# Optimization experiments

Measured on AMD Instinct MI355X. Metric: run time of the kernel, lower is better.

Reference implementation:

```python
import jax, jax.numpy as jnp
import numpy as np

B, S, DIM = 4, 3968, 512
H, HD = 8, 64
CHUNK, NPM, MEM = 496, 32, 1024  # MEM == NPM + 2*CHUNK (required by module's EMA update broadcast)


def _lin(k, din, dout):
    kw, kb = jax.random.split(k)
    w = jax.random.normal(kw, (din, dout), jnp.float32) / np.sqrt(din)
    b = jax.random.normal(kb, (dout,), jnp.float32) * 0.01
    return w, b


def setup_inputs() -> dict:
    key = jax.random.key(0)
    ks = jax.random.split(key, 12)
    inp = {}
    inp["x"] = jax.random.normal(ks[0], (B, S, DIM), jnp.float32)
    inp["persistent_memory"] = jax.random.normal(ks[1], (NPM, DIM), jnp.float32)
    # outer query projection
    inp["Wq_out"], inp["bq_out"] = _lin(ks[2], DIM, DIM)
    # NeuralMemory projections
    inp["mk_w"], inp["mk_b"] = _lin(ks[3], DIM, DIM)
    inp["mv_w"], inp["mv_b"] = _lin(ks[4], DIM, DIM)
    inp["mq_w"], inp["mq_b"] = _lin(ks[5], DIM, DIM)
    # TitanAttention (standard MHA: q/k/v to H*HD, out proj back to DIM)
    inp["aq_w"], inp["aq_b"] = _lin(ks[6], DIM, H * HD)
    inp["ak_w"], inp["ak_b"] = _lin(ks[7], DIM, H * HD)
    inp["av_w"], inp["av_b"] = _lin(ks[8], DIM, H * HD)
    inp["ao_w"], inp["ao_b"] = _lin(ks[9], H * HD, DIM)
    return inp


def reference(x, persistent_memory, Wq_out, bq_out,
              mk_w, mk_b, mv_w, mv_b, mq_w, mq_b,
              aq_w, aq_b, ak_w, ak_b, av_w, av_b, ao_w, ao_b):
    Bn, Sn, D = x.shape
    nch = Sn // CHUNK
    inv_sqrt_d = 1.0 / np.sqrt(D).astype(np.float32)
    inv_sqrt_hd = 1.0 / np.sqrt(HD).astype(np.float32)

    def retrieve(mem, q):
        # mem: [B, MEM, D], q: [B, L, D]
        qp = q @ mq_w + mq_b
        k = mem @ mk_w + mk_b
        v = mem @ mv_w + mv_b
        sc = jnp.einsum('bqd,bmd->bqm', qp, k) * inv_sqrt_d
        a = jax.nn.softmax(sc, axis=-1)
        return jnp.einsum('bqm,bmd->bqd', a, v)

    def mha(t):
        # t: [B, L, D] -> [B, L, D]; dropout inactive (eval)
        Bm, L, _ = t.shape
        q = (t @ aq_w + aq_b).reshape(Bm, L, H, HD)
        k = (t @ ak_w + ak_b).reshape(Bm, L, H, HD)
        v = (t @ av_w + av_b).reshape(Bm, L, H, HD)
        sc = jnp.einsum('bqhd,bkhd->bhqk', q, k) * inv_sqrt_hd
        a = jax.nn.softmax(sc, axis=-1)
        o = jnp.einsum('bhqk,bkhd->bqhd', a, v).reshape(Bm, L, H * HD)
        return o @ ao_w + ao_b

    pm = jnp.broadcast_to(persistent_memory[None], (Bn, NPM, D))
    chunks = x.reshape(Bn, nch, CHUNK, D).transpose(1, 0, 2, 3)  # [nch, B, C, D]
    mem0 = jnp.zeros((Bn, MEM, D), x.dtype)

    def step(mem, chunk):
        query = chunk @ Wq_out + bq_out
        hist = retrieve(mem, query)                              # [B, C, D]
        combined = jnp.concatenate([pm, hist, chunk], axis=1)    # [B, MEM, D]
        attended = mha(combined)
        mem2 = 0.9 * mem + 0.1 * attended                        # EMA update
        mout = retrieve(mem2, attended)
        out = (attended * mout)[:, -CHUNK:]                      # keep last chunk slice
        return mem2, out

    _, outs = jax.lax.scan(step, mem0, chunks)                   # outs: [nch, B, C, D]
    return outs.transpose(1, 0, 2, 3).reshape(Bn, Sn, D)
```

## Files before the change

kernel.cpp:

```cpp
#include <hip/hip_runtime.h>
#include <hip/hip_fp16.h>


typedef __attribute__((ext_vector_type(8))) short short8;
typedef __attribute__((ext_vector_type(4))) float f32x4;

static __device__ __forceinline__ unsigned short f32_bf16(float f) {
  unsigned int u = __float_as_uint(f);
  u += 0x7FFFu + ((u >> 16) & 1u);
  return (unsigned short)(u >> 16);
}
static __device__ __forceinline__ unsigned pk(float lo, float hi) {
  return (unsigned)f32_bf16(lo) | ((unsigned)f32_bf16(hi) << 16);
}

template<int BM, int BN, int ATY, int BTY, int CTY, bool GUARD, bool BIAS>
__global__ __launch_bounds__(256) void gemm2(
    const void* __restrict__ Ap, long long Asb, long long Ash, int Ars,
    const void* __restrict__ Bp, long long Bsb, long long Bsh, int Brs,
    void* __restrict__ Cp, long long Csb, long long Csh, int Crs,
    void* __restrict__ Cp2, int csplit, void* __restrict__ Cp3,
    const float* __restrict__ bias, float scale, int M, int Kdim, int Hh)
{
  constexpr int LDP = 72;
  constexpr int WN = (BN >= 128) ? 2 : (BM >= 128 ? 1 : 2);
  constexpr int WM = 4 / WN;
  constexpr int MI = BM / (WM * 16);
  constexpr int NI = BN / (WN * 16);
  constexpr int AP = BM / 32;
  constexpr int BP = BN / 32;

  __shared__ unsigned short As[2][BM][LDP];
  __shared__ unsigned short Bs[2][BN][LDP];

  const int tid  = threadIdx.x;
  const int lane = tid & 63;
  const int w    = tid >> 6;
  const int wm   = w / WN, wn = w % WN;
  const int z    = blockIdx.z;
  const int zb   = z / Hh, zh = z - zb * Hh;
  const int m0   = blockIdx.x * BM;
  const int n0   = blockIdx.y * BN;
  const int lrow = lane & 15;
  const int lkB  = (lane >> 4) * 8;
  const int srow = tid >> 3;
  const int scol = (tid & 7) * 8;

  const float*          Af  = (const float*)Ap          + zb * Asb + zh * Ash;
  const unsigned short* Ahp = (const unsigned short*)Ap + zb * Asb + zh * Ash;
  const float*          Bf  = (const float*)Bp          + zb * Bsb + zh * Bsh;
  const unsigned short* Bhp = (const unsigned short*)Bp + zb * Bsb + zh * Bsh;

  float4 afl[AP][2]; uint4 ahl[AP];
  float4 bfl[BP][2]; uint4 bhl[BP];

  auto loadT = [&](int k0) {
    #pragma unroll
    for (int p = 0; p < AP; ++p) {
      const int row = srow + p * 32;
      const bool ok = !GUARD || (m0 + row) < M;
      if constexpr (ATY == 0) {
        if (ok) {
          const float* s = Af + (long long)(m0 + row) * Ars + k0 + scol;
          afl[p][0] = *(const float4*)s;
          afl[p][1] = *(const float4*)(s + 4);
        } else {
          afl[p][0] = make_float4(0.f,0.f,0.f,0.f);
          afl[p][1] = make_float4(0.f,0.f,0.f,0.f);
        }
      } else {
        ahl[p] = ok ? *(const uint4*)(Ahp + (long long)(m0 + row) * Ars + k0 + scol)
                    : make_uint4(0u,0u,0u,0u);
      }
    }
    #pragma unroll
    for (int p = 0; p < BP; ++p) {
      const int row = srow + p * 32;
      if constexpr (BTY == 0) {
        const float* s = Bf + (long long)(n0 + row) * Brs + k0 + scol;
        bfl[p][0] = *(const float4*)s;
        bfl[p][1] = *(const float4*)(s + 4);
      } else {
        bhl[p] = *(const uint4*)(Bhp + (long long)(n0 + row) * Brs + k0 + scol);
      }
    }
  };
  auto writeT = [&](int buf) {
    #pragma unroll
    for (int p = 0; p < AP; ++p) {
      const int row = srow + p * 32;
      uint4 u;
      if constexpr (ATY == 0) {
        u.x = pk(afl[p][0].x, afl[p][0].y); u.y = pk(afl[p][0].z, afl[p][0].w);
        u.z = pk(afl[p][1].x, afl[p][1].y); u.w = pk(afl[p][1].z, afl[p][1].w);
      } else u = ahl[p];
      *(uint4*)(&As[buf][row][scol]) = u;
    }
    #pragma unroll
    for (int p = 0; p < BP; ++p) {
      const int row = srow + p * 32;
      uint4 u;
      if constexpr (BTY == 0) {
        u.x = pk(bfl[p][0].x, bfl[p][0].y); u.y = pk(bfl[p][0].z, bfl[p][0].w);
        u.z = pk(bfl[p][1].x, bfl[p][1].y); u.w = pk(bfl[p][1].z, bfl[p][1].w);
      } else u = bhl[p];
      *(uint4*)(&Bs[buf][row][scol]) = u;
    }
  };

  f32x4 acc[MI][NI] = {};

  loadT(0);
  writeT(0);
  __syncthreads();

  const int NT = Kdim >> 6;
  int cur = 0;
  for (int t = 0; t < NT; ++t) {
    const bool more = (t + 1) < NT;
    if (more) loadT((t + 1) << 6);

    short8 a8[MI][2], b8[NI][2];
    #pragma unroll
    for (int mi = 0; mi < MI; ++mi) {
      const unsigned short* r = &As[cur][wm * (MI * 16) + mi * 16 + lrow][lkB];
      a8[mi][0] = *(const short8*)r;
      a8[mi][1] = *(const short8*)(r + 32);
    }
    #pragma unroll
    for (int ni = 0; ni < NI; ++ni) {
      const unsigned short* r = &Bs[cur][wn * (NI * 16) + ni * 16 + lrow][lkB];
      b8[ni][0] = *(const short8*)r;
      b8[ni][1] = *(const short8*)(r + 32);
    }
    #pragma unroll
    for (int kk = 0; kk < 2; ++kk)
      #pragma unroll
      for (int mi = 0; mi < MI; ++mi)
        #pragma unroll
        for (int ni = 0; ni < NI; ++ni)
          acc[mi][ni] = __builtin_amdgcn_mfma_f32_16x16x32_bf16(a8[mi][kk], b8[ni][kk], acc[mi][ni], 0, 0, 0);

    if (more) writeT(cur ^ 1);
    __syncthreads();
    cur ^= 1;
  }

  float*          Cf  = (float*)Cp          + zb * Csb + zh * Csh;
  unsigned short* Chn = (unsigned short*)Cp + zb * Csb + zh * Csh;
  unsigned short* Ch2 = (unsigned short*)Cp2;
  unsigned short* Kb3 = (unsigned short*)Cp3;
  const bool trside = (CTY == 4 || CTY == 5) ? (n0 >= csplit) : false;

  #pragma unroll
  for (int ni = 0; ni < NI; ++ni) {
    const int col = n0 + wn * (NI * 16) + ni * 16 + lrow;
    const float bv = BIAS ? bias[col] : 0.0f;
    #pragma unroll
    for (int mi = 0; mi < MI; ++mi) {
      const int rbase = m0 + wm * (MI * 16) + mi * 16 + ((lane >> 4) << 2);
      if constexpr (CTY == 5) {
        ushort4 vt;
        #pragma unroll
        for (int r = 0; r < 4; ++r) {
          const int row = rbase + r;
          const float proj = acc[mi][ni][r] * scale + bv;
          const long long midx = (long long)row * Crs + col;
          const float v = 0.9f * Cf[midx] + 0.1f * proj;
          Cf[midx] = v;
          if (!trside) Kb3[(long long)row * 512 + col] = f32_bf16(v);
          else ((unsigned short*)&vt)[r] = f32_bf16(v);
        }
        if (trside)
          *(ushort4*)(&Ch2[(long long)(rbase >> 10) * 524288
                           + (long long)(col - csplit) * 1024 + (rbase & 1023)]) = vt;
      } else if constexpr (CTY == 6) {
        const float* ATTp = (const float*)Cp2;
        float* Of = (float*)Cp;
        #pragma unroll
        for (int r = 0; r < 4; ++r) {
          const int row = rbase + r;
          if (row < M) {
            const float v = acc[mi][ni][r] * scale;
            const float a = ATTp[((long long)zb * 1024 + 528 + row) * 512 + col];
            Of[((long long)zb * 3968 + (long long)csplit * 496 + row) * 512 + col] = v * a;
          }
        }
      } else if constexpr (CTY == 7) {
        #pragma unroll
        for (int r = 0; r < 4; ++r) {
          const int row = rbase + r;
          const float v = acc[mi][ni][r] * scale + bv;
          Cf[(long long)row * Crs + col] = v;
          Kb3[(long long)row * 512 + col] = f32_bf16(v);
        }
      } else if (trside) {
        ushort4 v;
        v.x = f32_bf16(acc[mi][ni][0] * scale + bv);
        v.y = f32_bf16(acc[mi][ni][1] * scale + bv);
        v.z = f32_bf16(acc[mi][ni][2] * scale + bv);
        v.w = f32_bf16(acc[mi][ni][3] * scale + bv);
        *(ushort4*)(&Ch2[(long long)(rbase >> 10) * 524288
                         + (long long)(col - csplit) * 1024 + (rbase & 1023)]) = v;
      } else {
        #pragma unroll
        for (int r = 0; r < 4; ++r) {
          const int row = rbase + r;
          if (!GUARD || row < M) {
            const float v = acc[mi][ni][r] * scale + bv;
            if constexpr (CTY == 0)      Cf [(long long)row * Crs + col] = v;
            else                         Chn[(long long)row * Crs + col] = f32_bf16(v);
          }
        }
      }
    }
  }
}

__global__ __launch_bounds__(256) void flash_mha(
    const unsigned short* __restrict__ QK, const unsigned short* __restrict__ Vt,
    unsigned short* __restrict__ OH)
{
  __shared__ unsigned short Ks[128][72];
  __shared__ unsigned short Vs[64][136];
  __shared__ unsigned short Ps[64][136];

  const int tid = threadIdx.x, lane = tid & 63, w = tid >> 6;
  const int f = blockIdx.x;
  const int xcd = f & 7, j = f >> 3;
  const int bh = xcd + 8 * (j >> 4);
  const int qt = j & 15;
  const int b = bh >> 3, h = bh & 7;
  const int q0 = qt * 64;
  const unsigned short* Qp = QK + (long long)b * 1048576 + h * 64;
  const unsigned short* Kp = Qp + 512;
  const unsigned short* Vp = Vt + (long long)b * 524288 + (long long)(h * 64) * 1024;
  unsigned short* Op = OH + (long long)b * 524288 + h * 64;

  const int lr = lane & 15, g = lane >> 4, lk = g * 8;
  const int wq = w * 16;

  short8 qb[2];
  qb[0] = *(const short8*)(Qp + (long long)(q0 + wq + lr) * 1024 + lk);
  qb[1] = *(const short8*)(Qp + (long long)(q0 + wq + lr) * 1024 + 32 + lk);

  const int krow = tid >> 1, kcol = (tid & 1) * 32;
  const int vrow = tid >> 2, vcol = (tid & 3) * 32;

  uint4 kl[4], vl[4];
  auto loadKV = [&](int kt) {
    #pragma unroll
    for (int jj = 0; jj < 4; ++jj)
      kl[jj] = *(const uint4*)(Kp + (long long)(kt * 128 + krow) * 1024 + kcol + jj * 8);
    #pragma unroll
    for (int jj = 0; jj < 4; ++jj)
      vl[jj] = *(const uint4*)(Vp + (long long)vrow * 1024 + kt * 128 + vcol + jj * 8);
  };
  auto writeKV = [&]() {
    #pragma unroll
    for (int jj = 0; jj < 4; ++jj) *(uint4*)(&Ks[krow][kcol + jj * 8]) = kl[jj];
    #pragma unroll
    for (int jj = 0; jj < 4; ++jj) *(uint4*)(&Vs[vrow][vcol + jj * 8]) = vl[jj];
  };

  loadKV(0); writeKV();
  __syncthreads();

  f32x4 acc[4] = {};
  float m = -1e30f, l = 0.f;

  for (int kt = 0; kt < 8; ++kt) {
    const bool more = kt < 7;
    if (more) loadKV(kt + 1);

    f32x4 s[8] = {};
    #pragma unroll
    for (int ks = 0; ks < 2; ++ks)
      #pragma unroll
      for (int ni = 0; ni < 8; ++ni) {
        const short8 ka = *(const short8*)(&Ks[ni * 16 + lr][ks * 32 + lk]);
        s[ni] = __builtin_amdgcn_mfma_f32_16x16x32_bf16(ka, qb[ks], s[ni], 0, 0, 0);
      }

    #pragma unroll
    for (int ni = 0; ni < 8; ++ni)
      #pragma unroll
      for (int r = 0; r < 4; ++r) s[ni][r] *= 0.125f;
    f32x4 rv = s[0];
    #pragma unroll
    for (int ni = 1; ni < 8; ++ni)
      #pragma unroll
      for (int r = 0; r < 4; ++r) rv[r] = fmaxf(rv[r], s[ni][r]);
    float rm = fmaxf(fmaxf(rv[0], rv[1]), fmaxf(rv[2], rv[3]));
    rm = fmaxf(rm, __shfl_xor(rm, 16));
    rm = fmaxf(rm, __shfl_xor(rm, 32));

    const float mn = fmaxf(m, rm);
    const float al = __expf(m - mn);
    m = mn;
    f32x4 lv; lv[0] = lv[1] = lv[2] = lv[3] = 0.f;
    #pragma unroll
    for (int ni = 0; ni < 8; ++ni)
      #pragma unroll
      for (int r = 0; r < 4; ++r) { s[ni][r] = __expf(s[ni][r] - m); lv[r] += s[ni][r]; }
    float ls = (lv[0] + lv[1]) + (lv[2] + lv[3]);
    ls += __shfl_xor(ls, 16);
    ls += __shfl_xor(ls, 32);
    l = l * al + ls;
    #pragma unroll
    for (int nd = 0; nd < 4; ++nd)
      #pragma unroll
      for (int r = 0; r < 4; ++r) acc[nd][r] *= al;

    #pragma unroll
    for (int ni = 0; ni < 8; ++ni) {
      unsigned lo, hi;
      asm("v_cvt_pk_bf16_f32 %0, %1, %2" : "=v"(lo) : "v"(s[ni][0]), "v"(s[ni][1]));
      asm("v_cvt_pk_bf16_f32 %0, %1, %2" : "=v"(hi) : "v"(s[ni][2]), "v"(s[ni][3]));
      *(uint2*)(&Ps[wq + lr][ni * 16 + (g << 2)]) = make_uint2(lo, hi);
    }

    #pragma unroll
    for (int ks2 = 0; ks2 < 4; ++ks2) {
      const short8 pb = *(const short8*)(&Ps[wq + lr][ks2 * 32 + lk]);
      #pragma unroll
      for (int nd = 0; nd < 4; ++nd) {
        const short8 va = *(const short8*)(&Vs[nd * 16 + lr][ks2 * 32 + lk]);
        acc[nd] = __builtin_amdgcn_mfma_f32_16x16x32_bf16(va, pb, acc[nd], 0, 0, 0);
      }
    }

    __syncthreads();
    if (more) { writeKV(); __syncthreads(); }
  }

  unsigned short (*Os)[72] = (unsigned short (*)[72])&Ks[0][0];
  const float inv = 1.0f / l;
  #pragma unroll
  for (int nd = 0; nd < 4; ++nd) {
    const float a0 = acc[nd][0] * inv, a1 = acc[nd][1] * inv;
    const float a2 = acc[nd][2] * inv, a3 = acc[nd][3] * inv;
    unsigned lo, hi;
    asm("v_cvt_pk_bf16_f32 %0, %1, %2" : "=v"(lo) : "v"(a0), "v"(a1));
    asm("v_cvt_pk_bf16_f32 %0, %1, %2" : "=v"(hi) : "v"(a2), "v"(a3));
    *(uint2*)(&Os[wq + lr][nd * 16 + (g << 2)]) = make_uint2(lo, hi);
  }
  __syncthreads();
  const int orow = tid >> 2, ocol = (tid & 3) * 16;
  const uint4 u0 = *(const uint4*)(&Os[orow][ocol]);
  const uint4 u1 = *(const uint4*)(&Os[orow][ocol + 8]);
  *(uint4*)(Op + (long long)(q0 + orow) * 512 + ocol) = u0;
  *(uint4*)(Op + (long long)(q0 + orow) * 512 + ocol + 8) = u1;
}

struct TP7 { const float* s[7]; unsigned short* d[7]; };
__global__ __launch_bounds__(256) void transpose7(TP7 tp)
{
  __shared__ float tile[32][33];
  const float* in = tp.s[blockIdx.z];
  unsigned short* out = tp.d[blockIdx.z];
  const int c0 = blockIdx.x * 32, r0 = blockIdx.y * 32;
  const int xx = threadIdx.x & 31, ys = threadIdx.x >> 5;
  #pragma unroll
  for (int yy = ys; yy < 32; yy += 8)
    tile[yy][xx] = in[(long long)(r0 + yy) * 512 + c0 + xx];
  __syncthreads();
  #pragma unroll
  for (int yy = ys; yy < 32; yy += 8)
    out[(long long)(c0 + yy) * 512 + r0 + xx] = f32_bf16(tile[xx][yy]);
}

__global__ __launch_bounds__(256) void softmax_rows_bf(
    const float* __restrict__ buf, unsigned short* __restrict__ obuf,
    int rowsPerZ, long long zStride)
{
  const int gr   = blockIdx.x * 4 + (threadIdx.x >> 6);
  const int lane = threadIdx.x & 63;
  const int z = gr / rowsPerZ;
  const int i = gr - z * rowsPerZ;
  const float* pf = buf + (long long)z * zStride + (long long)i * 1024 + lane * 16;
  float v[16];
  #pragma unroll
  for (int j = 0; j < 4; ++j) {
    const float4 f = ((const float4*)pf)[j];
    v[4*j+0] = f.x; v[4*j+1] = f.y; v[4*j+2] = f.z; v[4*j+3] = f.w;
  }
  float mx = v[0];
  #pragma unroll
  for (int j = 1; j < 16; ++j) mx = fmaxf(mx, v[j]);
  #pragma unroll
  for (int d = 32; d; d >>= 1) mx = fmaxf(mx, __shfl_xor(mx, d));
  float s = 0.0f;
  #pragma unroll
  for (int j = 0; j < 16; ++j) { v[j] = __expf(v[j] - mx); s += v[j]; }
  #pragma unroll
  for (int d = 32; d; d >>= 1) s += __shfl_xor(s, d);
  const float inv = 1.0f / s;
  unsigned short* ph = obuf + (long long)z * zStride + (long long)i * 1024 + lane * 16;
  unsigned uu[8];
  #pragma unroll
  for (int j = 0; j < 8; ++j) uu[j] = pk(v[2*j] * inv, v[2*j+1] * inv);
  ((uint4*)ph)[0] = make_uint4(uu[0], uu[1], uu[2], uu[3]);
  ((uint4*)ph)[1] = make_uint4(uu[4], uu[5], uu[6], uu[7]);
}

__global__ __launch_bounds__(256) void copy_pm_bf(const float* __restrict__ pm, unsigned short* __restrict__ comb)
{
  const int idx = blockIdx.x * 256 + threadIdx.x;
  const int b = idx >> 11, e = idx & 2047;
  const int row = e >> 6, d8 = (e & 63) * 8;
  const float* s = pm + row * 512 + d8;
  const float4 f0 = *(const float4*)s;
  const float4 f1 = *(const float4*)(s + 4);
  uint4 u; u.x = pk(f0.x, f0.y); u.y = pk(f0.z, f0.w); u.z = pk(f1.x, f1.y); u.w = pk(f1.z, f1.w);
  *(uint4*)(comb + (long long)b * 524288 + row * 512 + d8) = u;
}

__global__ __launch_bounds__(256) void copy_chunk_bf(const float* __restrict__ x, unsigned short* __restrict__ comb, int ci)
{
  const int idx = blockIdx.x * 256 + threadIdx.x;
  const int b = idx / 31744, e = idx % 31744;
  const int row = e >> 6, d8 = (e & 63) * 8;
  const float* s = x + ((long long)b * 3968 + ci * 496 + row) * 512 + d8;
  const float4 f0 = *(const float4*)s;
  const float4 f1 = *(const float4*)(s + 4);
  uint4 u; u.x = pk(f0.x, f0.y); u.y = pk(f0.z, f0.w); u.z = pk(f1.x, f1.y); u.w = pk(f1.z, f1.w);
  *(uint4*)(comb + (long long)b * 524288 + (528 + row) * 512 + d8) = u;
}

__global__ __launch_bounds__(256) void init_kv(const float* __restrict__ mkb, const float* __restrict__ mvb,
                                               float* __restrict__ master, unsigned short* __restrict__ Kb)
{
  const int idx = blockIdx.x * 256 + threadIdx.x;
  const int c4 = (idx & 255) * 4;
  const long long row = idx >> 8;
  const float4 v = *(const float4*)((c4 < 512) ? (mkb + c4) : (mvb + c4 - 512));
  *(float4*)(master + row * 1024 + c4) = v;
  if (c4 < 512) {
    ushort4 h; h.x = f32_bf16(v.x); h.y = f32_bf16(v.y); h.z = f32_bf16(v.z); h.w = f32_bf16(v.w);
    *(ushort4*)(Kb + row * 512 + c4) = h;
  }
}

__global__ __launch_bounds__(256) void init_vt(const float* __restrict__ mvb, unsigned short* __restrict__ VT)
{
  const int idx = blockIdx.x * 256 + threadIdx.x;
  const int k8 = (idx & 127) * 8;
  const int d  = (idx >> 7) & 511;
  const int b  = idx >> 16;
  const unsigned short hv = f32_bf16(mvb[d]);
  const ushort4 h4 = make_ushort4(hv, hv, hv, hv);
  unsigned short* dst = VT + (long long)b * 524288 + (long long)d * 1024 + k8;
  *(ushort4*)dst = h4; *(ushort4*)(dst + 4) = h4;
}

__global__ __launch_bounds__(256) void fuse_bias(const float* __restrict__ bq, const float* __restrict__ mq,
                                                 const float* __restrict__ mqb, float* __restrict__ bqm)
{
  const int c = blockIdx.x * 256 + threadIdx.x;
  float s = mqb[c];
  for (int j = 0; j < 512; ++j) s += bq[j] * mq[j * 512 + c];
  bqm[c] = s;
}

extern "C" void kernel_launch(void* const* d_in, const int* in_sizes, int n_in,
                              void* d_out, int out_size, void* d_ws, size_t ws_size,
                              hipStream_t stream)
{
  (void)in_sizes; (void)n_in; (void)out_size; (void)ws_size;
  const float* x   = (const float*)d_in[0];
  const float* pm  = (const float*)d_in[1];
  const float* Wq  = (const float*)d_in[2];
  const float* bq  = (const float*)d_in[3];
  const float* mkw = (const float*)d_in[4];
  const float* mkb = (const float*)d_in[5];
  const float* mvw = (const float*)d_in[6];
  const float* mvb = (const float*)d_in[7];
  const float* mqw = (const float*)d_in[8];
  const float* mqb = (const float*)d_in[9];
  const float* aqw = (const float*)d_in[10];
  const float* aqb = (const float*)d_in[11];
  const float* akw = (const float*)d_in[12];
  const float* akb = (const float*)d_in[13];
  const float* avw = (const float*)d_in[14];
  const float* avb = (const float*)d_in[15];
  const float* aow = (const float*)d_in[16];
  const float* aob = (const float*)d_in[17];
  float* out = (float*)d_out;

  char* wsp = (char*)d_ws;
  size_t off = 0;
  auto alloc = [&](size_t b) -> void* { void* p = wsp + off; off += (b + 255) & ~(size_t)255; return p; };

  unsigned short* WTmq = (unsigned short*)alloc(524288);
  unsigned short* WKV  = (unsigned short*)alloc(1048576);
  unsigned short* WQKV = (unsigned short*)alloc(1572864);
  unsigned short* WTao = (unsigned short*)alloc(524288);
  unsigned short* Wqm  = (unsigned short*)alloc(524288);
  float* bkv  = (float*)alloc(4096);
  float* bqkv = (float*)alloc(6144);
  float* bqm  = (float*)alloc(2048);
  float*          master = (float*)alloc(16777216);
  unsigned short* Kb   = (unsigned short*)alloc(4194304);
  unsigned short* VT   = (unsigned short*)alloc(4194304);
  unsigned short* VTm  = (unsigned short*)alloc(4194304);
  unsigned short* QP1  = (unsigned short*)alloc(16252928);
  unsigned short* QP   = (unsigned short*)alloc(2031616);
  unsigned short* comb = (unsigned short*)alloc(4194304);
  unsigned short* QKb  = (unsigned short*)alloc(8388608);
  unsigned short* OH   = (unsigned short*)alloc(4194304);
  float*          ATT  = (float*)alloc(8388608);
  unsigned short* ATTb = (unsigned short*)alloc(4194304);
  float*          SC   = (float*)alloc(8126464);
  unsigned short* SCb  = (unsigned short*)alloc(4063232);

  const long long XBS = 2031616, BS = 524288, QBS = 253952;
  const long long SCB = 507904;
  const float sr = 0.044194173824159216f;

  TP7 tp;
  tp.s[0] = mqw; tp.d[0] = WTmq;
  tp.s[1] = mkw; tp.d[1] = WKV;
  tp.s[2] = mvw; tp.d[2] = WKV + 262144;
  tp.s[3] = aqw; tp.d[3] = WQKV;
  tp.s[4] = akw; tp.d[4] = WQKV + 262144;
  tp.s[5] = avw; tp.d[5] = WQKV + 524288;
  tp.s[6] = aow; tp.d[6] = WTao;
  transpose7<<<dim3(16,16,7),256,0,stream>>>(tp);
  gemm2<64,64,1,0,2,false,false><<<dim3(8,8,1),256,0,stream>>>(
    WTmq, 0, 0, 512, Wq, 0, 0, 512, Wqm, 0, 0, 512,
    nullptr, 0, nullptr, nullptr, 1.0f, 512, 512, 1);
  fuse_bias<<<2,256,0,stream>>>(bq, mqw, mqb, bqm);
  gemm2<128,64,0,1,2,false,true><<<dim3(124,8,1),256,0,stream>>>(
    x, 0, 0, 512, Wqm, 0, 0, 512,
    QP1, 0, 0, 512, nullptr, 0, nullptr, bqm, 1.0f, 15872, 512, 1);
  hipMemcpyAsync(bkv,        mkb, 2048, hipMemcpyDeviceToDevice, stream);
  hipMemcpyAsync(bkv  + 512, mvb, 2048, hipMemcpyDeviceToDevice, stream);
  hipMemcpyAsync(bqkv,       aqb, 2048, hipMemcpyDeviceToDevice, stream);
  hipMemcpyAsync(bqkv + 512, akb, 2048, hipMemcpyDeviceToDevice, stream);
  hipMemcpyAsync(bqkv +1024, avb, 2048, hipMemcpyDeviceToDevice, stream);
  init_kv<<<4096,256,0,stream>>>(mkb, mvb, master, Kb);
  init_vt<<<1024,256,0,stream>>>(mvb, VT);
  copy_pm_bf<<<32,256,0,stream>>>(pm, comb);

  for (int ci = 0; ci < 8; ++ci) {
    copy_chunk_bf<<<496,256,0,stream>>>(x, comb, ci);

    gemm2<64,64,1,1,0,true,false><<<dim3(8,16,4),256,0,stream>>>(
      QP1 + (long long)ci * 253952, XBS, 0, 512, Kb, BS, 0, 512,
      SC, SCB, 0, 1024, nullptr, 0, nullptr, nullptr, sr, 496, 512, 1);
    softmax_rows_bf<<<496,256,0,stream>>>(SC, SCb, 496, SCB);
    gemm2<64,64,1,1,2,true,false><<<dim3(8,8,4),256,0,stream>>>(
      SCb, SCB, 0, 1024, VT, BS, 0, 1024,
      comb + 32 * 512, BS, 0, 512, nullptr, 0, nullptr, nullptr, 1.0f, 496, 1024, 1);

    gemm2<128,64,1,1,4,false,true><<<dim3(32,24,1),256,0,stream>>>(
      comb, 0, 0, 512, WQKV, 0, 0, 512,
      QKb, 0, 0, 1024, VTm, 1024, nullptr, bqkv, 1.0f, 4096, 512, 1);
    flash_mha<<<512,256,0,stream>>>(QKb, VTm, OH);
    gemm2<128,64,1,1,7,false,true><<<dim3(32,8,1),256,0,stream>>>(
      OH, 0, 0, 512, WTao, 0, 0, 512,
      ATT, 0, 0, 512, nullptr, 0, ATTb, aob, 1.0f, 4096, 512, 1);

    gemm2<128,64,1,1,5,false,true><<<dim3(32,16,1),256,0,stream>>>(
      ATTb, 0, 0, 512, WKV, 0, 0, 512,
      master, 0, 0, 1024, VT, 512, Kb, bkv, 1.0f, 4096, 512, 1);

    gemm2<64,64,1,1,2,true,true><<<dim3(8,8,4),256,0,stream>>>(
      ATTb + 528 * 512, BS, 0, 512, WTmq, 0, 0, 512,
      QP, QBS, 0, 512, nullptr, 0, nullptr, mqb, 1.0f, 496, 512, 1);
    gemm2<64,64,1,1,0,true,false><<<dim3(8,16,4),256,0,stream>>>(
      QP, QBS, 0, 512, Kb, BS, 0, 512,
      SC, SCB, 0, 1024, nullptr, 0, nullptr, nullptr, sr, 496, 512, 1);
    softmax_rows_bf<<<496,256,0,stream>>>(SC, SCb, 496, SCB);
    gemm2<64,64,1,1,6,true,false><<<dim3(8,8,4),256,0,stream>>>(
      SCb, SCB, 0, 1024, VT, BS, 0, 1024,
      out, 0, 0, 512, ATT, ci, nullptr, nullptr, 1.0f, 496, 1024, 1);
  }
}
```

Baseline: 1.336 ms.

## Load K/V MFMA fragments directly from global memory in flash attention, drop LDS staging

The flash attention kernel no longer stages K and V tiles through shared memory with block-wide barriers. Each wave now loads its K and V MFMA operands straight from global memory into registers. The P scratch buffer is shrunk to an unpadded 64x128 array with an XOR swizzle to avoid bank conflicts. This removes the LDS round trip and the __syncthreads per tile, but each of the four waves now fetches the full K/V tile separately, which quadruples global/L2 traffic and raises register pressure, with no prefetch overlap.

New measurement: 1.435 ms. 7.4% more time.

```diff
diff --git a/kernel.cpp b/kernel.cpp
--- a/kernel.cpp
+++ b/kernel.cpp
@@ -221,9 +221,7 @@
     const unsigned short* __restrict__ QK, const unsigned short* __restrict__ Vt,
     unsigned short* __restrict__ OH)
 {
-  __shared__ unsigned short Ks[128][72];
-  __shared__ unsigned short Vs[64][136];
-  __shared__ unsigned short Ps[64][136];
+  __shared__ unsigned short Ps[64][128];
 
   const int tid = threadIdx.x, lane = tid & 63, w = tid >> 6;
   const int f = blockIdx.x;
@@ -239,48 +237,39 @@
 
   const int lr = lane & 15, g = lane >> 4, lk = g * 8;
   const int wq = w * 16;
+  const int swz = (lr & 7) << 4;
+  char* prow = (char*)&Ps[0][0] + (wq + lr) * 256;
 
   short8 qb[2];
   qb[0] = *(const short8*)(Qp + (long long)(q0 + wq + lr) * 1024 + lk);
   qb[1] = *(const short8*)(Qp + (long long)(q0 + wq + lr) * 1024 + 32 + lk);
 
-  const int krow = tid >> 1, kcol = (tid & 1) * 32;
-  const int vrow = tid >> 2, vcol = (tid & 3) * 32;
-
-  uint4 kl[4], vl[4];
-  auto loadKV = [&](int kt) {
-    #pragma unroll
-    for (int jj = 0; jj < 4; ++jj)
-      kl[jj] = *(const uint4*)(Kp + (long long)(kt * 128 + krow) * 1024 + kcol + jj * 8);
-    #pragma unroll
-    for (int jj = 0; jj < 4; ++jj)
-      vl[jj] = *(const uint4*)(Vp + (long long)vrow * 1024 + kt * 128 + vcol + jj * 8);
-  };
-  auto writeKV = [&]() {
-    #pragma unroll
-    for (int jj = 0; jj < 4; ++jj) *(uint4*)(&Ks[krow][kcol + jj * 8]) = kl[jj];
-    #pragma unroll
-    for (int jj = 0; jj < 4; ++jj) *(uint4*)(&Vs[vrow][vcol + jj * 8]) = vl[jj];
-  };
-
-  loadKV(0); writeKV();
-  __syncthreads();
-
   f32x4 acc[4] = {};
   float m = -1e30f, l = 0.f;
 
+  #pragma unroll 1
   for (int kt = 0; kt < 8; ++kt) {
-    const bool more = kt < 7;
-    if (more) loadKV(kt + 1);
+    const unsigned short* kbase = Kp + (long long)(kt * 128 + lr) * 1024 + lk;
+    short8 kf[2][8];
+    #pragma unroll
+    for (int ni = 0; ni < 8; ++ni) {
+      kf[0][ni] = *(const short8*)(kbase + ni * 16384);
+      kf[1][ni] = *(const short8*)(kbase + ni * 16384 + 32);
+    }
+    const unsigned short* vbase = Vp + (long long)lr * 1024 + kt * 128 + lk;
+    short8 vf[4][4];
+    #pragma unroll
+    for (int ks2 = 0; ks2 < 4; ++ks2)
+      #pragma unroll
+      for (int nd = 0; nd < 4; ++nd)
+        vf[ks2][nd] = *(const short8*)(vbase + nd * 16384 + ks2 * 32);
 
     f32x4 s[8] = {};
     #pragma unroll
     for (int ks = 0; ks < 2; ++ks)
       #pragma unroll
-      for (int ni = 0; ni < 8; ++ni) {
-        const short8 ka = *(const short8*)(&Ks[ni * 16 + lr][ks * 32 + lk]);
-        s[ni] = __builtin_amdgcn_mfma_f32_16x16x32_bf16(ka, qb[ks], s[ni], 0, 0, 0);
-      }
+      for (int ni = 0; ni < 8; ++ni)
+        s[ni] = __builtin_amdgcn_mfma_f32_16x16x32_bf16(kf[ks][ni], qb[ks], s[ni], 0, 0, 0);
 
     #pragma unroll
     for (int ni = 0; ni < 8; ++ni)
@@ -317,24 +306,18 @@
       unsigned lo, hi;
       asm("v_cvt_pk_bf16_f32 %0, %1, %2" : "=v"(lo) : "v"(s[ni][0]), "v"(s[ni][1]));
       asm("v_cvt_pk_bf16_f32 %0, %1, %2" : "=v"(hi) : "v"(s[ni][2]), "v"(s[ni][3]));
-      *(uint2*)(&Ps[wq + lr][ni * 16 + (g << 2)]) = make_uint2(lo, hi);
+      *(uint2*)(prow + ((32 * ni + 8 * g) ^ swz)) = make_uint2(lo, hi);
     }
 
     #pragma unroll
     for (int ks2 = 0; ks2 < 4; ++ks2) {
-      const short8 pb = *(const short8*)(&Ps[wq + lr][ks2 * 32 + lk]);
-      #pragma unroll
-      for (int nd = 0; nd < 4; ++nd) {
-        const short8 va = *(const short8*)(&Vs[nd * 16 + lr][ks2 * 32 + lk]);
-        acc[nd] = __builtin_amdgcn_mfma_f32_16x16x32_bf16(va, pb, acc[nd], 0, 0, 0);
-      }
-    }
-
-    __syncthreads();
-    if (more) { writeKV(); __syncthreads(); }
-  }
-
-  unsigned short (*Os)[72] = (unsigned short (*)[72])&Ks[0][0];
+      const short8 pb = *(const short8*)(prow + ((64 * ks2 + 16 * g) ^ swz));
+      #pragma unroll
+      for (int nd = 0; nd < 4; ++nd)
+        acc[nd] = __builtin_amdgcn_mfma_f32_16x16x32_bf16(vf[ks2][nd], pb, acc[nd], 0, 0, 0);
+    }
+  }
+
   const float inv = 1.0f / l;
   #pragma unroll
   for (int nd = 0; nd < 4; ++nd) {
@@ -343,14 +326,16 @@
     unsigned lo, hi;
     asm("v_cvt_pk_bf16_f32 %0, %1, %2" : "=v"(lo) : "v"(a0), "v"(a1));
     asm("v_cvt_pk_bf16_f32 %0, %1, %2" : "=v"(hi) : "v"(a2), "v"(a3));
-    *(uint2*)(&Os[wq + lr][nd * 16 + (g << 2)]) = make_uint2(lo, hi);
+    *(uint2*)(prow + ((32 * nd + 8 * g) ^ swz)) = make_uint2(lo, hi);
   }
   __syncthreads();
-  const int orow = tid >> 2, ocol = (tid & 3) * 16;
-  const uint4 u0 = *(const uint4*)(&Os[orow][ocol]);
-  const uint4 u1 = *(const uint4*)(&Os[orow][ocol + 8]);
-  *(uint4*)(Op + (long long)(q0 + orow) * 512 + ocol) = u0;
-  *(uint4*)(Op + (long long)(q0 + orow) * 512 + ocol + 8) = u1;
+  const int orow = tid >> 2, oc = (tid & 3) * 32;
+  char* orp = (char*)&Ps[0][0] + orow * 256;
+  const int oswz = (orow & 7) << 4;
+  const uint4 u0 = *(const uint4*)(orp + (oc ^ oswz));
+  const uint4 u1 = *(const uint4*)(orp + ((oc + 16) ^ oswz));
+  *(uint4*)(Op + (long long)(q0 + orow) * 512 + (tid & 3) * 16) = u0;
+  *(uint4*)(Op + (long long)(q0 + orow) * 512 + (tid & 3) * 16 + 8) = u1;
 }
 
 struct TP7 { const float* s[7]; unsigned short* d[7]; };
```
